# Performance work log

Measured on AMD Instinct MI355X. Metric: run time of the kernel, lower is better.

The kernel has to match this reference:

```python
import jax, jax.numpy as jnp
import numpy as np

ATT_WIDTH = 512  # attention_width from init

def _band_mask(T, width, dtype):
    # tf.matrix_band_part(ones, width//2, (width-1)//2): keep i-j<=lower and j-i<=upper
    lower = width // 2
    upper = (width - 1) // 2
    i = jnp.arange(T)[:, None]
    j = jnp.arange(T)[None, :]
    keep = (i - j <= lower) & (j - i <= upper)
    return keep.astype(dtype)

def setup_inputs() -> dict:
    key = jax.random.key(0)
    k1, k2, k3, k4 = jax.random.split(key, 4)
    B, T, H, D = 8, 2048, 1024, 1024
    scale = 1.0 / np.sqrt(H)  # keep activations sane
    return {
        "inputs": jax.random.normal(k1, (B, T, H), dtype=jnp.float32),
        "WQ": jax.random.normal(k2, (H, D), dtype=jnp.float32) * scale,
        "WK": jax.random.normal(k3, (H, D), dtype=jnp.float32) * scale,
        "WV": jax.random.normal(k4, (H, D), dtype=jnp.float32) * scale,
    }

def reference(inputs, WQ, WK, WV) -> jnp.ndarray:
    B, T, H = inputs.shape
    D = WQ.shape[1]
    scale = jnp.asarray(D, inputs.dtype) ** 0.5
    q = jnp.einsum('bth,hd->btd', inputs, WQ)
    k = jnp.einsum('bth,hd->btd', inputs, WK)
    v = jnp.einsum('bth,hd->btd', inputs, WV)
    score = jnp.einsum('bqd,bkd->bqk', q, k) / scale  # [B,T,T]
    # NOTE: original multiplies score by the 0/1 band mask BEFORE softmax
    # (masked entries become 0, not -inf). Faithful reproduction.
    local = _band_mask(T, ATT_WIDTH, score.dtype)
    score = score * local[None, :, :]
    attn = jax.nn.softmax(score, axis=-1)
    return jnp.einsum('bqk,bkd->bqd', attn, v)
```

## Files before the change

kernel.cpp:

```cpp
#include <hip/hip_runtime.h>
#include <hip/hip_bf16.h>
#include <stdint.h>

typedef __attribute__((ext_vector_type(8))) short bf16x8;
typedef __attribute__((ext_vector_type(4))) short short4v;
typedef __attribute__((ext_vector_type(4))) float f32x4;

#define DEV static __device__ __forceinline__

DEV float bf2f(short u) {
    union { float f; uint32_t i; } c; c.i = ((uint32_t)(uint16_t)u) << 16; return c.f;
}
DEV short f2bf(float f) {
    union { float f; uint32_t i; } c; c.f = f;
    uint32_t i = c.i;
    uint32_t r = i + 0x7FFFu + ((i >> 16) & 1u);
    return (short)(r >> 16);
}

DEV void gload_lds16(const short* g, short* l) {
    __builtin_amdgcn_global_load_lds(
        (const __attribute__((address_space(1))) void*)g,
        (__attribute__((address_space(3))) void*)l,
        16, 0, 0);
}

__global__ __launch_bounds__(256)
void cvt_f32_bf16(const float* __restrict__ in, short* __restrict__ out) {
    long i = ((long)blockIdx.x * 256 + threadIdx.x) * 8;
    float4 a = *(const float4*)&in[i];
    float4 b = *(const float4*)&in[i + 4];
    bf16x8 o;
    o[0] = f2bf(a.x); o[1] = f2bf(a.y); o[2] = f2bf(a.z); o[3] = f2bf(a.w);
    o[4] = f2bf(b.x); o[5] = f2bf(b.y); o[6] = f2bf(b.z); o[7] = f2bf(b.w);
    *(bf16x8*)&out[i] = o;
}

__global__ __launch_bounds__(256)
void transpose_w(const float* __restrict__ W, short* __restrict__ Wt) {
    const int HD = 1024;
    __shared__ float tile[32][33];
    int bx = blockIdx.x, by = blockIdx.y;
    int tx = threadIdx.x & 31, ty = threadIdx.x >> 5;
    #pragma unroll
    for (int r = ty; r < 32; r += 8)
        tile[r][tx] = W[(long)(by * 32 + r) * HD + bx * 32 + tx];
    __syncthreads();
    #pragma unroll
    for (int r = ty; r < 32; r += 8)
        Wt[(long)(bx * 32 + r) * HD + by * 32 + tx] = f2bf(tile[tx][r]);
}

__global__ __launch_bounds__(256)
void reduce_mt(const float* __restrict__ Mpart, short* __restrict__ MTb) {
    const long SL = 1024L * 1024;
    long i = ((long)blockIdx.x * 256 + threadIdx.x) * 8;
    float s[8];
    #pragma unroll
    for (int j = 0; j < 8; ++j) s[j] = 0.f;
    #pragma unroll
    for (int sl = 0; sl < 4; ++sl) {
        float4 a = *(const float4*)&Mpart[sl * SL + i];
        float4 b = *(const float4*)&Mpart[sl * SL + i + 4];
        s[0] += a.x; s[1] += a.y; s[2] += a.z; s[3] += a.w;
        s[4] += b.x; s[5] += b.y; s[6] += b.z; s[7] += b.w;
    }
    bf16x8 o;
    #pragma unroll
    for (int j = 0; j < 8; ++j) o[j] = f2bf(s[j]);
    *(bf16x8*)&MTb[i] = o;
}


DEV void stage_half(const short* __restrict__ src, int ld, short* dst, int tid) {
    int rr = tid >> 3;
    int cs = ((tid & 7) ^ (rr & 7)) << 3;
    short* d = dst + ((tid >> 6) << 9);
    gload_lds16(src + (long)rr * ld + cs, d);
    gload_lds16(src + (long)(rr + 64) * ld + cs, d + 4096);
}

DEV bf16x8 ld_frag(const short* half, int rowbase, int ks, int lane) {
    int row = rowbase + (lane & 15);
    int idx = (row << 6) + ks * 32 + ((lane >> 4) << 3);
    idx ^= (lane & 7) << 3;
    return *(const bf16x8*)&half[idx];
}

#define SCHED0 __builtin_amdgcn_sched_barrier(0)
#define SBAR do { SCHED0; __builtin_amdgcn_s_barrier(); SCHED0; } while (0)
#define LGK(n) do { asm volatile("s_waitcnt lgkmcnt(" #n ")" ::: "memory"); SCHED0; } while (0)
#define VM(n)  do { asm volatile("s_waitcnt vmcnt(" #n ")" ::: "memory"); SCHED0; } while (0)
#define PRIO1 __builtin_amdgcn_s_setprio(1)
#define PRIO0 __builtin_amdgcn_s_setprio(0)

#define READ_A(HP, QM)                                                          \
    do { _Pragma("unroll") for (int iq = 0; iq < 4; ++iq)                       \
         _Pragma("unroll") for (int ks = 0; ks < 2; ++ks)                       \
             ra[iq][ks] = ld_frag(HP, (QM)*64 + iq*16, ks, lane); } while (0)

#define READ_B(HP, QN)                                                          \
    do { _Pragma("unroll") for (int jn = 0; jn < 2; ++jn)                       \
         _Pragma("unroll") for (int ks = 0; ks < 2; ++ks)                       \
             rb[QN][jn][ks] = ld_frag(HP, wn1*64 + (QN)*32 + jn*16, ks, lane); } while (0)

#define MFMA_Q(QM, QN)                                                          \
    do { _Pragma("unroll") for (int iq = 0; iq < 4; ++iq)                       \
         _Pragma("unroll") for (int jn = 0; jn < 2; ++jn)                       \
         _Pragma("unroll") for (int ks = 0; ks < 2; ++ks)                       \
             acc[(QM)*4+iq][(QN)*2+jn] = __builtin_amdgcn_mfma_f32_16x16x32_bf16( \
                 ra[iq][ks], rb[QN][jn][ks], acc[(QM)*4+iq][(QN)*2+jn], 0,0,0); } while (0)

template<int EPI>
__global__ __launch_bounds__(512, 2)
void gemm256(const short* __restrict__ Abase, const short* __restrict__ Bbase,
             void* __restrict__ o0, void* __restrict__ o1, void* __restrict__ o2,
             const float* __restrict__ Crow, const float* __restrict__ Vsum)
{
    const int T = 2048, HD = 1024;
    __shared__ __align__(16) short lds[2][2][2][8192];

    const int tid  = threadIdx.x;
    const int lane = tid & 63;
    const int w    = tid >> 6;
    const int wm   = w >> 2;
    const int wn   = w & 3;
    const int wn1  = wn & 1;

    int m0, n0, klo, khi, ldA, ldB, bz;
    const short *A, *B;
    if (EPI == 0) {
        int p = (int)blockIdx.x + 8 * (int)blockIdx.y;
        int lid = (p & 7) * 64 + (p >> 3);
        m0 = (lid >> 3) * 256; n0 = (lid & 7) * 256;
        klo = 0; khi = 1024; ldA = HD; ldB = HD; bz = 0;
        A = Abase; B = Bbase;
    } else if (EPI == 1) {
        int p = (int)blockIdx.x + 3 * ((int)blockIdx.y + 8 * (int)blockIdx.z);
        bz = p & 7; int rem = p >> 3;
        int mb = rem / 3, kb = mb + rem % 3 - 1;
        if (kb < 0 || kb > 7) return;
        m0 = mb * 256; n0 = kb * 256;
        klo = 0; khi = 1024; ldA = HD; ldB = HD;
        A = Abase + (long)bz * T * HD; B = Bbase + (long)bz * T * HD;
    } else if (EPI == 2) {
        int p = (int)blockIdx.x + 4 * ((int)blockIdx.y + 8 * (int)blockIdx.z);
        bz = p & 7; int rem = p >> 3;
        int mb = rem / 4;
        m0 = mb * 256; n0 = (rem % 4) * 256;
        klo = max(m0 - 256, 0); khi = min(m0 + 512, T);
        ldA = T; ldB = T;
        A = Abase + (long)bz * T * T; B = Bbase + (long)bz * HD * T;
    } else {
        m0 = blockIdx.y * 256; n0 = blockIdx.x * 256;
        klo = (int)blockIdx.z * 256; khi = klo + 256;
        ldA = HD; ldB = HD; bz = 0;
        A = Abase; B = Bbase;
    }

    const short* Asrc = A + (long)m0 * ldA + klo;
    const short* Bsrc = B + (long)n0 * ldB + klo;
    const short* hA0 = &lds[0][0][wm][0];
    const short* hA1 = &lds[1][0][wm][0];
    const short* hB0 = &lds[0][1][wn >> 1][0];
    const short* hB1 = &lds[1][1][wn >> 1][0];

    auto stA = [&](int bf, int hf, int t) {
        stage_half(Asrc + (long)hf * 128 * ldA + t * 64, ldA, (short*)&lds[bf][0][hf][0], tid); };
    auto stB = [&](int bf, int hf, int t) {
        stage_half(Bsrc + (long)hf * 128 * ldB + t * 64, ldB, (short*)&lds[bf][1][hf][0], tid); };

    f32x4 acc[8][4];
    #pragma unroll
    for (int i = 0; i < 8; ++i)
        #pragma unroll
        for (int j = 0; j < 4; ++j) { acc[i][j][0]=0.f; acc[i][j][1]=0.f; acc[i][j][2]=0.f; acc[i][j][3]=0.f; }
    bf16x8 ra[4][2];
    bf16x8 rb[2][2][2];

    const int NT = (khi - klo) >> 6;

    stB(0,0,0); stB(0,1,0); stA(0,0,0); stA(0,1,0); stB(1,0,1); stB(1,1,1);
    SCHED0; VM(4); SBAR;
    READ_B(hB0, 0); SCHED0;

    #pragma unroll 1
    for (int i = 0; i < NT/2 - 1; ++i) {
        int t1 = 2*i+1, t2 = 2*i+2, t3 = 2*i+3;
        SBAR; READ_A(hA0,0); SCHED0; READ_B(hB0,1); SCHED0; stA(1,0,t1);
        LGK(4); PRIO1; MFMA_Q(0,0); PRIO0; SCHED0;
        SBAR; stA(1,1,t1); LGK(0); PRIO1; MFMA_Q(0,1); PRIO0; SCHED0;
        SBAR; READ_A(hA0,1); SCHED0; stB(0,0,t2); LGK(0);
        PRIO1; MFMA_Q(1,0); PRIO0; SCHED0; VM(2); SCHED0;
        SBAR; READ_B(hB1,0); SCHED0; stB(0,1,t2);
        PRIO1; MFMA_Q(1,1); PRIO0; SCHED0;
        SBAR; READ_A(hA1,0); SCHED0; READ_B(hB1,1); SCHED0; stA(0,0,t2);
        LGK(4); PRIO1; MFMA_Q(0,0); PRIO0; SCHED0;
        SBAR; stA(0,1,t2); LGK(0); PRIO1; MFMA_Q(0,1); PRIO0; SCHED0;
        SBAR; READ_A(hA1,1); SCHED0; stB(1,0,t3); LGK(0);
        PRIO1; MFMA_Q(1,0); PRIO0; SCHED0; VM(2); SCHED0;
        SBAR; READ_B(hB0,0); SCHED0; stB(1,1,t3);
        PRIO1; MFMA_Q(1,1); PRIO0; SCHED0;
    }
    {
        int t1 = NT - 1;
        SBAR; READ_A(hA0,0); SCHED0; READ_B(hB0,1); SCHED0; stA(1,0,t1);
        LGK(4); PRIO1; MFMA_Q(0,0); PRIO0; SCHED0;
        SBAR; stA(1,1,t1); LGK(0); PRIO1; MFMA_Q(0,1); PRIO0; SCHED0;
        SBAR; READ_A(hA0,1); SCHED0; LGK(0);
        PRIO1; MFMA_Q(1,0); PRIO0; SCHED0; VM(0); SCHED0;
        SBAR; READ_B(hB1,0); SCHED0; PRIO1; MFMA_Q(1,1); PRIO0; SCHED0;
        SBAR; READ_A(hA1,0); SCHED0; READ_B(hB1,1); SCHED0;
        LGK(4); PRIO1; MFMA_Q(0,0); PRIO0; SCHED0;
        SBAR; LGK(0); PRIO1; MFMA_Q(0,1); PRIO0; SCHED0;
        SBAR; READ_A(hA1,1); SCHED0; LGK(0); PRIO1; MFMA_Q(1,0); PRIO0; SCHED0;
        SBAR; PRIO1; MFMA_Q(1,1); PRIO0; SCHED0;
    }

    const int fr = lane & 15, fq = lane >> 4;
    const int rbase = m0 + wm * 128, cbase = n0 + wn * 64;

    if (EPI == 0) {
        const int wsel = n0 >> 10;
        if (wsel == 0) {
            short* dst = (short*)o0;
            #pragma unroll
            for (int mi = 0; mi < 8; ++mi)
                #pragma unroll
                for (int ni = 0; ni < 4; ++ni)
                    #pragma unroll
                    for (int r = 0; r < 4; ++r) {
                        int row = rbase + mi * 16 + fq * 4 + r;
                        int col = cbase + ni * 16 + fr;
                        dst[(long)row * HD + col] = f2bf(acc[mi][ni][r]);
                    }
        } else {
            short* Vt = (short*)o2;
            #pragma unroll
            for (int mi = 0; mi < 8; ++mi)
                #pragma unroll
                for (int ni = 0; ni < 4; ++ni) {
                    int col  = (cbase + ni * 16 + fr) & 1023;
                    int row0 = rbase + mi * 16 + fq * 4;
                    int b = row0 >> 11, t = row0 & 2047;
                    short4v v;
                    #pragma unroll
                    for (int r = 0; r < 4; ++r) v[r] = f2bf(acc[mi][ni][r]);
                    *(short4v*)&Vt[((long)b * HD + col) * T + t] = v;
                }
        }
    } else if (EPI == 1) {
        short* S = (short*)o0 + (long)bz * T * T;
        #pragma unroll
        for (int mi = 0; mi < 8; ++mi)
            #pragma unroll
            for (int ni = 0; ni < 4; ++ni)
                #pragma unroll
                for (int r = 0; r < 4; ++r) {
                    int i = rbase + mi * 16 + fq * 4 + r;
                    int j = cbase + ni * 16 + fr;
                    bool keep = (i - j <= 256) && (j - i <= 255);
                    S[(long)i * T + j] = f2bf(keep ? acc[mi][ni][r] * (1.f/32.f) : 0.f);
                }
    } else if (EPI == 2) {
        float* out = (float*)o0;
        #pragma unroll
        for (int mi = 0; mi < 8; ++mi)
            #pragma unroll
            for (int r = 0; r < 4; ++r) {
                int i = rbase + mi * 16 + fq * 4 + r;
                float ci = Crow[bz * T + i];
                #pragma unroll
                for (int ni = 0; ni < 4; ++ni) {
                    int col = cbase + ni * 16 + fr;
                    out[((long)bz * T + i) * HD + col] = acc[mi][ni][r] + ci * Vsum[bz * HD + col];
                }
            }
    } else {
        float* dst = (float*)o0 + (long)blockIdx.z * HD * HD;
        #pragma unroll
        for (int mi = 0; mi < 8; ++mi)
            #pragma unroll
            for (int ni = 0; ni < 4; ++ni)
                #pragma unroll
                for (int r = 0; r < 4; ++r) {
                    int row = rbase + mi * 16 + fq * 4 + r;
                    int col = cbase + ni * 16 + fr;
                    dst[(long)row * HD + col] = acc[mi][ni][r];
                }
    }
}

__global__ __launch_bounds__(256)
void softmax_band(short* __restrict__ S, float* __restrict__ Crow) {
    const int T = 2048;
    int wid = (int)blockIdx.x * 4 + (threadIdx.x >> 6);
    int lane = threadIdx.x & 63;
    int b = wid >> 11, t = wid & 2047;
    int mb = t >> 7;
    int tlo = max(mb - 2, 0) * 128;
    int thi = min(mb + 2, 15) * 128 + 128;
    int nvec = (thi - tlo) >> 3;
    short* row = S + ((long)b * T + t) * T + tlo;

    bool h0 = lane < nvec;
    bool h1 = lane + 64 < nvec;
    bf16x8 v0, v1;
    float f0[8], f1[8];
    float m = 0.f;
    if (h0) {
        v0 = *(const bf16x8*)&row[lane * 8];
        #pragma unroll
        for (int j = 0; j < 8; ++j) { f0[j] = bf2f(v0[j]); m = fmaxf(m, f0[j]); }
    }
    if (h1) {
        v1 = *(const bf16x8*)&row[(lane + 64) * 8];
        #pragma unroll
        for (int j = 0; j < 8; ++j) { f1[j] = bf2f(v1[j]); m = fmaxf(m, f1[j]); }
    }
    #pragma unroll
    for (int o = 32; o; o >>= 1) m = fmaxf(m, __shfl_xor(m, o));

    float e0[8], e1[8];
    float sum = 0.f;
    if (h0) {
        #pragma unroll
        for (int j = 0; j < 8; ++j) { e0[j] = __expf(f0[j] - m); sum += e0[j]; }
    }
    if (h1) {
        #pragma unroll
        for (int j = 0; j < 8; ++j) { e1[j] = __expf(f1[j] - m); sum += e1[j]; }
    }
    #pragma unroll
    for (int o = 32; o; o >>= 1) sum += __shfl_xor(sum, o);
    float em = __expf(-m);
    sum += (float)(2048 - nvec * 8) * em;
    float inv = 1.f / sum;
    float c = em * inv;

    if (h0) {
        #pragma unroll
        for (int j = 0; j < 8; ++j) v0[j] = f2bf(e0[j] * inv - c);
        *(bf16x8*)&row[lane * 8] = v0;
    }
    if (h1) {
        #pragma unroll
        for (int j = 0; j < 8; ++j) v1[j] = f2bf(e1[j] * inv - c);
        *(bf16x8*)&row[(lane + 64) * 8] = v1;
    }
    if (lane == 0) Crow[wid] = c;
}

__global__ __launch_bounds__(256)
void vsum_rows(const short* __restrict__ Vt, float* __restrict__ Vsum) {
    int rowid = (int)blockIdx.x * 4 + (threadIdx.x >> 6);
    int lane = threadIdx.x & 63;
    const short* r = Vt + (long)rowid * 2048;
    float s = 0.f;
    #pragma unroll
    for (int v = 0; v < 4; ++v) {
        bf16x8 x = *(const bf16x8*)&r[(lane + v * 64) * 8];
        #pragma unroll
        for (int j = 0; j < 8; ++j) s += bf2f(x[j]);
    }
    #pragma unroll
    for (int o = 32; o; o >>= 1) s += __shfl_xor(s, o);
    if (lane == 0) Vsum[rowid] = s;
}

extern "C" void kernel_launch(void* const* d_in, const int* in_sizes, int n_in,
                              void* d_out, int out_size, void* d_ws, size_t ws_size,
                              hipStream_t stream) {
    const int B = 8, T = 2048, H = 1024, D = 1024;
    const long MT = (long)B * T;

    const float* X  = (const float*)d_in[0];
    const float* WQ = (const float*)d_in[1];
    const float* WK = (const float*)d_in[2];
    const float* WV = (const float*)d_in[3];
    float* out = (float*)d_out;

    char* ws = (char*)d_ws;
    size_t off = 0;
    auto alloc = [&](size_t bytes) {
        char* p = ws + off;
        off += (bytes + 255) & ~(size_t)255;
        return p;
    };
    short* Xb    = (short*)alloc(MT * H * 2);
    short* WQb   = (short*)alloc((long)H * D * 2);
    short* WKb   = (short*)alloc((long)H * D * 2);
    short* Bfuse = (short*)alloc(2L * D * H * 2);
    short* MTb   = Bfuse;
    short* WVt   = Bfuse + (long)D * H;
    float* Mpart = (float*)alloc(4L * D * H * 4);
    short* Gb    = (short*)alloc(MT * D * 2);
    short* Vt    = (short*)alloc((long)B * D * T * 2);
    short* S     = (short*)alloc((long)B * T * T * 2);
    float* Crow  = (float*)alloc(MT * 4);
    float* Vsum  = (float*)alloc((long)B * D * 4);
    if (off > ws_size) return;

    cvt_f32_bf16<<<(int)(MT * H / 2048), 256, 0, stream>>>(X, Xb);
    cvt_f32_bf16<<<512, 256, 0, stream>>>(WQ, WQb);
    cvt_f32_bf16<<<512, 256, 0, stream>>>(WK, WKb);
    transpose_w<<<dim3(32, 32), 256, 0, stream>>>(WV, WVt);

    gemm256<3><<<dim3(4, 4, 4), 512, 0, stream>>>(WKb, WQb, Mpart, nullptr, nullptr, nullptr, nullptr);
    reduce_mt<<<512, 256, 0, stream>>>(Mpart, MTb);

    gemm256<0><<<dim3(8, 64, 1), 512, 0, stream>>>(Xb, Bfuse, Gb, nullptr, Vt, nullptr, nullptr);

    vsum_rows<<<(int)(B * D / 4), 256, 0, stream>>>(Vt, Vsum);

    gemm256<1><<<dim3(3, 8, B), 512, 0, stream>>>(Gb, Xb, S, nullptr, nullptr, nullptr, nullptr);

    softmax_band<<<(int)(MT / 4), 256, 0, stream>>>(S, Crow);

    gemm256<2><<<dim3(4, 8, B), 512, 0, stream>>>(S, Vt, out, nullptr, nullptr, Crow, Vsum);
}
```

Baseline: 212.5 us.

## Double-buffer A fragments in registers to prefetch LDS reads ahead of MFMAs

Splits the A-fragment registers into two sets (ra0/ra1) so the next half-tile's A fragments are read from LDS one phase earlier. The reads overlap with the MFMAs of the current phase, and the waitcnt thresholds are relaxed so MFMAs start before every LDS read has completed. This is meant to hide LDS read latency inside the GEMM main loop. It adds 8 VGPRs of bf16x8 per thread, which may pressure register allocation under launch_bounds(512,2), and the lgkmcnt counts must exactly match the issue order to stay correct.

```diff
diff --git a/kernel.cpp b/kernel.cpp
--- a/kernel.cpp
+++ b/kernel.cpp
@@ -94,22 +94,25 @@
 #define PRIO1 __builtin_amdgcn_s_setprio(1)
 #define PRIO0 __builtin_amdgcn_s_setprio(0)
 
-#define READ_A(HP, QM)                                                          \
+#define READ_A0(HP)                                                             \
     do { _Pragma("unroll") for (int iq = 0; iq < 4; ++iq)                       \
          _Pragma("unroll") for (int ks = 0; ks < 2; ++ks)                       \
-             ra[iq][ks] = ld_frag(HP, (QM)*64 + iq*16, ks, lane); } while (0)
-
+             ra0[iq][ks] = ld_frag(HP, iq*16, ks, lane); } while (0)
+#define READ_A1(HP)                                                             \
+    do { _Pragma("unroll") for (int iq = 0; iq < 4; ++iq)                       \
+         _Pragma("unroll") for (int ks = 0; ks < 2; ++ks)                       \
+             ra1[iq][ks] = ld_frag(HP, 64 + iq*16, ks, lane); } while (0)
 #define READ_B(HP, QN)                                                          \
     do { _Pragma("unroll") for (int jn = 0; jn < 2; ++jn)                       \
          _Pragma("unroll") for (int ks = 0; ks < 2; ++ks)                       \
              rb[QN][jn][ks] = ld_frag(HP, wn1*64 + (QN)*32 + jn*16, ks, lane); } while (0)
 
-#define MFMA_Q(QM, QN)                                                          \
+#define MFMA_Q(QM, QN, RA)                                                      \
     do { _Pragma("unroll") for (int iq = 0; iq < 4; ++iq)                       \
          _Pragma("unroll") for (int jn = 0; jn < 2; ++jn)                       \
          _Pragma("unroll") for (int ks = 0; ks < 2; ++ks)                       \
              acc[(QM)*4+iq][(QN)*2+jn] = __builtin_amdgcn_mfma_f32_16x16x32_bf16( \
-                 ra[iq][ks], rb[QN][jn][ks], acc[(QM)*4+iq][(QN)*2+jn], 0,0,0); } while (0)
+                 RA[iq][ks], rb[QN][jn][ks], acc[(QM)*4+iq][(QN)*2+jn], 0,0,0); } while (0)
 
 template<int EPI>
 __global__ __launch_bounds__(512, 2)
@@ -175,46 +178,49 @@
     for (int i = 0; i < 8; ++i)
         #pragma unroll
         for (int j = 0; j < 4; ++j) { acc[i][j][0]=0.f; acc[i][j][1]=0.f; acc[i][j][2]=0.f; acc[i][j][3]=0.f; }
-    bf16x8 ra[4][2];
+    bf16x8 ra0[4][2], ra1[4][2];
     bf16x8 rb[2][2][2];
 
     const int NT = (khi - klo) >> 6;
 
     stB(0,0,0); stB(0,1,0); stA(0,0,0); stA(0,1,0); stB(1,0,1); stB(1,1,1);
     SCHED0; VM(4); SBAR;
-    READ_B(hB0, 0); SCHED0;
+    READ_B(hB0, 0); SCHED0; READ_A0(hA0); SCHED0;
 
     #pragma unroll 1
     for (int i = 0; i < NT/2 - 1; ++i) {
         int t1 = 2*i+1, t2 = 2*i+2, t3 = 2*i+3;
-        SBAR; READ_A(hA0,0); SCHED0; READ_B(hB0,1); SCHED0; stA(1,0,t1);
-        LGK(4); PRIO1; MFMA_Q(0,0); PRIO0; SCHED0;
-        SBAR; stA(1,1,t1); LGK(0); PRIO1; MFMA_Q(0,1); PRIO0; SCHED0;
-        SBAR; READ_A(hA0,1); SCHED0; stB(0,0,t2); LGK(0);
-        PRIO1; MFMA_Q(1,0); PRIO0; SCHED0; VM(2); SCHED0;
-        SBAR; READ_B(hB1,0); SCHED0; stB(0,1,t2);
-        PRIO1; MFMA_Q(1,1); PRIO0; SCHED0;
-        SBAR; READ_A(hA1,0); SCHED0; READ_B(hB1,1); SCHED0; stA(0,0,t2);
-        LGK(4); PRIO1; MFMA_Q(0,0); PRIO0; SCHED0;
-        SBAR; stA(0,1,t2); LGK(0); PRIO1; MFMA_Q(0,1); PRIO0; SCHED0;
-        SBAR; READ_A(hA1,1); SCHED0; stB(1,0,t3); LGK(0);
-        PRIO1; MFMA_Q(1,0); PRIO0; SCHED0; VM(2); SCHED0;
-        SBAR; READ_B(hB0,0); SCHED0; stB(1,1,t3);
-        PRIO1; MFMA_Q(1,1); PRIO0; SCHED0;
+        SBAR; READ_B(hB0,1); SCHED0; READ_A1(hA0); SCHED0; stA(1,0,t1);
+        LGK(12); PRIO1; MFMA_Q(0,0,ra0); PRIO0; SCHED0;
+        SBAR; stA(1,1,t1);
+        LGK(8); PRIO1; MFMA_Q(0,1,ra0); PRIO0; SCHED0;
+        SBAR; stB(0,0,t2);
+        LGK(0); PRIO1; MFMA_Q(1,0,ra1); PRIO0; SCHED0; VM(2); SCHED0;
+        SBAR; READ_B(hB1,0); SCHED0; READ_A0(hA1); SCHED0; stB(0,1,t2);
+        PRIO1; MFMA_Q(1,1,ra1); PRIO0; SCHED0;
+        SBAR; READ_B(hB1,1); SCHED0; READ_A1(hA1); SCHED0; stA(0,0,t2);
+        LGK(12); PRIO1; MFMA_Q(0,0,ra0); PRIO0; SCHED0;
+        SBAR; stA(0,1,t2);
+        LGK(8); PRIO1; MFMA_Q(0,1,ra0); PRIO0; SCHED0;
+        SBAR; stB(1,0,t3);
+        LGK(0); PRIO1; MFMA_Q(1,0,ra1); PRIO0; SCHED0; VM(2); SCHED0;
+        SBAR; READ_B(hB0,0); SCHED0; READ_A0(hA0); SCHED0; stB(1,1,t3);
+        PRIO1; MFMA_Q(1,1,ra1); PRIO0; SCHED0;
     }
     {
         int t1 = NT - 1;
-        SBAR; READ_A(hA0,0); SCHED0; READ_B(hB0,1); SCHED0; stA(1,0,t1);
-        LGK(4); PRIO1; MFMA_Q(0,0); PRIO0; SCHED0;
-        SBAR; stA(1,1,t1); LGK(0); PRIO1; MFMA_Q(0,1); PRIO0; SCHED0;
-        SBAR; READ_A(hA0,1); SCHED0; LGK(0);
-        PRIO1; MFMA_Q(1,0); PRIO0; SCHED0; VM(0); SCHED0;
-        SBAR; READ_B(hB1,0); SCHED0; PRIO1; MFMA_Q(1,1); PRIO0; SCHED0;
-        SBAR; READ_A(hA1,0); SCHED0; READ_B(hB1,1); SCHED0;
-        LGK(4); PRIO1; MFMA_Q(0,0); PRIO0; SCHED0;
-        SBAR; LGK(0); PRIO1; MFMA_Q(0,1); PRIO0; SCHED0;
-        SBAR; READ_A(hA1,1); SCHED0; LGK(0); PRIO1; MFMA_Q(1,0); PRIO0; SCHED0;
-        SBAR; PRIO1; MFMA_Q(1,1); PRIO0; SCHED0;
+        SBAR; READ_B(hB0,1); SCHED0; READ_A1(hA0); SCHED0; stA(1,0,t1);
+        LGK(12); PRIO1; MFMA_Q(0,0,ra0); PRIO0; SCHED0;
+        SBAR; stA(1,1,t1);
+        LGK(8); PRIO1; MFMA_Q(0,1,ra0); PRIO0; SCHED0;
+        SBAR; LGK(0); PRIO1; MFMA_Q(1,0,ra1); PRIO0; SCHED0; VM(0); SCHED0;
+        SBAR; READ_B(hB1,0); SCHED0; READ_A0(hA1); SCHED0;
+        PRIO1; MFMA_Q(1,1,ra1); PRIO0; SCHED0;
+        SBAR; READ_B(hB1,1); SCHED0; READ_A1(hA1); SCHED0;
+        LGK(12); PRIO1; MFMA_Q(0,0,ra0); PRIO0; SCHED0;
+        SBAR; LGK(8); PRIO1; MFMA_Q(0,1,ra0); PRIO0; SCHED0;
+        SBAR; LGK(0); PRIO1; MFMA_Q(1,0,ra1); PRIO0; SCHED0;
+        SBAR; PRIO1; MFMA_Q(1,1,ra1); PRIO0; SCHED0;
     }
 
     const int fr = lane & 15, fq = lane >> 4;
```

New measurement: 451.7 us. 2.12x slower.
